# Kernel optimization log

Measured on AMD Instinct MI355X. Metric: run time of the kernel, lower is better.

Reference implementation:

```python
import jax, jax.numpy as jnp
import numpy as np

B, N, DIN, DOUT = 16, 256, 64, 64
TEMP = 2.0          # temperatures[0]
POOL_K = 0.5        # pool_ratios[0]
BN_EPS = 1e-5


def setup_inputs() -> dict:
    key = jax.random.key(0)
    ks = jax.random.split(key, 8)
    g = lambda i, shape: (jax.random.normal(ks[i], shape, jnp.float32) * 0.08)
    return {
        "x": jax.random.normal(ks[0], (B, N, DIN), jnp.float32),
        # GraphAttentionLayer params
        "W_att": g(1, (DIN, DOUT)), "b_att": jnp.zeros((DOUT,), jnp.float32),
        "att_w": g(2, (DOUT,)),                      # att_weight [DOUT,1] squeezed
        "W_pwa": g(3, (DIN, DOUT)), "b_pwa": jnp.zeros((DOUT,), jnp.float32),
        "W_pna": g(4, (DIN, DOUT)), "b_pna": jnp.zeros((DOUT,), jnp.float32),
        "bn_scale": jnp.ones((DOUT,), jnp.float32),
        "bn_bias": jnp.zeros((DOUT,), jnp.float32),
        # GraphPool params
        "pool_w": g(5, (DOUT,)), "pool_b": jnp.zeros((), jnp.float32),
    }


def reference(x, W_att, b_att, att_w, W_pwa, b_pwa, W_pna, b_pna,
              bn_scale, bn_bias, pool_w, pool_b):
    # --- GraphAttentionLayer (eval mode: dropout = identity) ---
    # pairwise node multiplication: [B, i, j, DIN]
    pm = x[:, :, None, :] * x[:, None, :, :]
    att = jnp.tanh(jnp.einsum('bijd,de->bije', pm, W_att) + b_att)   # [B,N,N,DOUT]
    logits = jnp.einsum('bije,e->bij', att, att_w) / TEMP            # [B,N,N]
    # torch softmax over dim=-2 of [B,i,j,1] == axis j (the aggregated axis)
    A = jax.nn.softmax(logits, axis=2)                               # [B,N,N]
    agg = jnp.einsum('bij,bjd->bid', A, x)                           # [B,N,DIN]
    h = (agg @ W_pwa + b_pwa) + (x @ W_pna + b_pna)                  # [B,N,DOUT]
    # BatchNorm1d eval with running_mean=0, running_var=1
    h = h * (bn_scale / jnp.sqrt(1.0 + BN_EPS)) + bn_bias
    h = jax.nn.selu(h)
    # --- GraphPool (eval mode: dropout = identity) ---
    scores = jax.nn.sigmoid(h @ pool_w + pool_b)                     # [B,N]
    k = max(int(N * POOL_K), 1)
    _, idx = jax.lax.top_k(scores, k)                                # [B,k]
    hw = h * scores[:, :, None]
    out = jnp.take_along_axis(hw, idx[:, :, None], axis=1)           # [B,k,DOUT]
    return out
```

## Files before the change

### kernel.cpp

```cpp
#include <hip/hip_runtime.h>
#include <hip/hip_bf16.h>
#include <math.h>

#define BB 16
#define NN 256
#define DD 64
#define KTOP 128

typedef short s16x8 __attribute__((ext_vector_type(8)));
typedef float f32x4 __attribute__((ext_vector_type(4)));

typedef union { s16x8 v; unsigned u[4]; } frag_u;
typedef union { __hip_bfloat162 b2; unsigned u; } cvu;

__device__ __forceinline__ float asf(unsigned u){ union{unsigned u;float f;}c; c.u=u; return c.f; }

__device__ __forceinline__ void split2(float v0, float v1, unsigned& hu, unsigned& lu) {
    cvu c; c.b2 = __float22bfloat162_rn(make_float2(v0, v1));
    unsigned h = c.u;
    float l0 = v0 - asf(h << 16);
    float l1 = v1 - asf(h & 0xffff0000u);
    c.b2 = __float22bfloat162_rn(make_float2(l0, l1));
    hu = h; lu = c.u;
}

__global__ __launch_bounds__(512, 6) void k_logits(
    const float* __restrict__ x, const float* __restrict__ W_att,
    const float* __restrict__ b_att, const float* __restrict__ att_w,
    float* __restrict__ U)
{
    const int ig = blockIdx.x;
    const int b  = blockIdx.y;
    const int tid = threadIdx.x;
    const int w = tid >> 6, lane = tid & 63;
    const int quad = lane >> 4, c16 = lane & 15;
    const int ibase = ig * 4;
    const int G = ig >> 3;
    const bool active = w < (8 - G);
    const int jb = (G + w) * 32;

    __shared__ s16x8 sB[2][2][4][2][64];
    __shared__ float sXi[4 * 64];
    __shared__ float sL[4][256];
    __shared__ float sBatt[64];
    __shared__ float sAww[64];

    if (tid < 256) sXi[tid] = x[(b * NN + ibase + (tid >> 6)) * DD + (tid & 63)];
    if (tid < 64) sBatt[tid] = b_att[tid];
    else if (tid < 128) sAww[tid - 64] = att_w[tid - 64];

    const float L2E2 = 2.8853900817779268f;

    float halfS;
    {
        float sa = 0.0f;
        #pragma unroll
        for (int mt = 0; mt < 4; ++mt) {
            float4 a4 = ((const float4*)att_w)[mt * 4 + quad];
            sa += (a4.x + a4.y) + (a4.z + a4.w);
        }
        sa += __shfl_xor(sa, 16);
        sa += __shfl_xor(sa, 32);
        halfS = 0.5f * sa;
    }

    const int bks = w >> 2, bmt = w & 3;

    frag_u Xh[2][2], Xl[2][2];
    if (active) {
        #pragma unroll
        for (int jt = 0; jt < 2; ++jt) {
            #pragma unroll
            for (int ks = 0; ks < 2; ++ks) {
                const float* xr = &x[(b * NN + jb + jt * 16 + c16) * DD + ks * 32 + quad * 8];
                float4 a0 = *(const float4*)xr;
                float4 a1 = *(const float4*)(xr + 4);
                split2(a0.x, a0.y, Xh[jt][ks].u[0], Xl[jt][ks].u[0]);
                split2(a0.z, a0.w, Xh[jt][ks].u[1], Xl[jt][ks].u[1]);
                split2(a1.x, a1.y, Xh[jt][ks].u[2], Xl[jt][ks].u[2]);
                split2(a1.z, a1.w, Xh[jt][ks].u[3], Xl[jt][ks].u[3]);
            }
        }
    }
    __syncthreads();

    {
        const float* xr = &sXi[0 * 64 + bks * 32 + quad * 8];
        float4 c0 = *(const float4*)xr;
        float4 c1 = *(const float4*)(xr + 4);
        float xiv[8] = {c0.x,c0.y,c0.z,c0.w,c1.x,c1.y,c1.z,c1.w};
        const float* wp = &W_att[(bks * 32 + quad * 8) * 64 + bmt * 16 + c16];
        frag_u bh, bl;
        split2(wp[0] * xiv[0], wp[64] * xiv[1], bh.u[0], bl.u[0]);
        split2(wp[128] * xiv[2], wp[192] * xiv[3], bh.u[1], bl.u[1]);
        split2(wp[256] * xiv[4], wp[320] * xiv[5], bh.u[2], bl.u[2]);
        split2(wp[384] * xiv[6], wp[448] * xiv[7], bh.u[3], bl.u[3]);
        sB[0][bks][bmt][0][lane] = bh.v;
        sB[0][bks][bmt][1][lane] = bl.v;
    }

    #pragma unroll
    for (int ii = 0; ii < 4; ++ii) {
        __syncthreads();

        if (ii < 3) {
            const float* xr = &sXi[(ii + 1) * 64 + bks * 32 + quad * 8];
            float4 c0 = *(const float4*)xr;
            float4 c1 = *(const float4*)(xr + 4);
            float xiv[8] = {c0.x,c0.y,c0.z,c0.w,c1.x,c1.y,c1.z,c1.w};
            const float* wp = &W_att[(bks * 32 + quad * 8) * 64 + bmt * 16 + c16];
            frag_u bh, bl;
            split2(wp[0] * xiv[0], wp[64] * xiv[1], bh.u[0], bl.u[0]);
            split2(wp[128] * xiv[2], wp[192] * xiv[3], bh.u[1], bl.u[1]);
            split2(wp[256] * xiv[4], wp[320] * xiv[5], bh.u[2], bl.u[2]);
            split2(wp[384] * xiv[6], wp[448] * xiv[7], bh.u[3], bl.u[3]);
            sB[(ii + 1) & 1][bks][bmt][0][lane] = bh.v;
            sB[(ii + 1) & 1][bks][bmt][1][lane] = bl.v;
        }

        if (active) {
            const int cur = ii & 1;
            float s0 = 0.0f, s1 = 0.0f;
            #pragma unroll
            for (int eth = 0; eth < 2; ++eth) {
                f32x4 acc[2][2];
                #pragma unroll
                for (int e2 = 0; e2 < 2; ++e2) {
                    f32x4 bi = *(const f32x4*)&sBatt[(eth * 2 + e2) * 16 + quad * 4];
                    acc[e2][0] = bi;
                    acc[e2][1] = bi;
                }
                #pragma unroll
                for (int ks = 0; ks < 2; ++ks) {
                    #pragma unroll
                    for (int e2 = 0; e2 < 2; ++e2) {
                        const int mt = eth * 2 + e2;
                        s16x8 ah = sB[cur][ks][mt][0][lane];
                        s16x8 al = sB[cur][ks][mt][1][lane];
                        #pragma unroll
                        for (int jt = 0; jt < 2; ++jt) {
                            acc[e2][jt] = __builtin_amdgcn_mfma_f32_16x16x32_bf16(ah, Xh[jt][ks].v, acc[e2][jt], 0, 0, 0);
                            acc[e2][jt] = __builtin_amdgcn_mfma_f32_16x16x32_bf16(al, Xh[jt][ks].v, acc[e2][jt], 0, 0, 0);
                            acc[e2][jt] = __builtin_amdgcn_mfma_f32_16x16x32_bf16(ah, Xl[jt][ks].v, acc[e2][jt], 0, 0, 0);
                        }
                    }
                }
                #pragma unroll
                for (int e2 = 0; e2 < 2; ++e2) {
                    const int mt = eth * 2 + e2;
                    f32x4 awwv = *(const f32x4*)&sAww[mt * 16 + quad * 4];
                    #pragma unroll
                    for (int r = 0; r < 4; ++r) {
                        {
                            float m = __builtin_amdgcn_exp2f(acc[e2][0][r] * L2E2);
                            s0 = fmaf(awwv[r], __builtin_amdgcn_rcpf(m + 1.0f), s0);
                        }
                        {
                            float m = __builtin_amdgcn_exp2f(acc[e2][1][r] * L2E2);
                            s1 = fmaf(awwv[r], __builtin_amdgcn_rcpf(m + 1.0f), s1);
                        }
                    }
                }
            }
            s0 += __shfl_xor(s0, 16);
            s0 += __shfl_xor(s0, 32);
            s1 += __shfl_xor(s1, 16);
            s1 += __shfl_xor(s1, 32);
            if (quad == 0) {
                sL[ii][jb + c16]      = halfS - s0;
                sL[ii][jb + 16 + c16] = halfS - s1;
            }
        }
    }
    __syncthreads();

    #pragma unroll
    for (int c = 0; c < 4; ++c) {
        float* Ur = &U[(b * NN + ibase + c) * NN];
        for (int j = ibase + tid; j < NN; j += 512) Ur[j] = sL[c][j];
    }
    {
        const int cnt = (NN - (ibase + 4)) * 4;
        for (int m = tid; m < cnt; m += 512) {
            int rr = ibase + 4 + (m >> 2);
            U[(b * NN + rr) * NN + ibase + (m & 3)] = sL[m & 3][rr];
        }
    }
}

__global__ __launch_bounds__(256) void k_soft(
    const float* __restrict__ x, const float* __restrict__ U,
    const float* __restrict__ Wpwa, const float* __restrict__ bpwa,
    const float* __restrict__ Wpna, const float* __restrict__ bpna,
    const float* __restrict__ bnsc, const float* __restrict__ bnbi,
    const float* __restrict__ poolw, const float* __restrict__ poolb,
    float* __restrict__ hbuf, float* __restrict__ scores)
{
    const int rg = blockIdx.x;
    const int b  = blockIdx.y;
    const int w = threadIdx.x >> 6, lane = threadIdx.x & 63;
    const int r = rg * 4 + w;

    __shared__ float sA[4][256];
    __shared__ float sAgg[4][64];
    __shared__ float sXi[4][64];

    const float* row = &U[(b * NN + r) * NN];
    float lg0 = row[lane], lg1 = row[lane + 64], lg2 = row[lane + 128], lg3 = row[lane + 192];
    float m = fmaxf(fmaxf(lg0, lg1), fmaxf(lg2, lg3));
    #pragma unroll
    for (int off = 32; off; off >>= 1) m = fmaxf(m, __shfl_xor(m, off));
    float e0 = __expf(lg0 - m), e1 = __expf(lg1 - m), e2 = __expf(lg2 - m), e3 = __expf(lg3 - m);
    float ssum = e0 + e1 + e2 + e3;
    #pragma unroll
    for (int off = 32; off; off >>= 1) ssum += __shfl_xor(ssum, off);
    float inv = 1.0f / ssum;
    sA[w][lane] = e0 * inv; sA[w][lane + 64] = e1 * inv;
    sA[w][lane + 128] = e2 * inv; sA[w][lane + 192] = e3 * inv;
    sXi[w][lane] = x[(b * NN + r) * DD + lane];
    __asm__ volatile("s_waitcnt lgkmcnt(0)" ::: "memory");

    float ag0 = 0.f, ag1 = 0.f, ag2 = 0.f, ag3 = 0.f;
    const float4* A4 = (const float4*)&sA[w][0];
    const float* xb = &x[(b * NN) * DD];
    #pragma unroll 8
    for (int jq = 0; jq < 64; ++jq) {
        float4 a = A4[jq];
        int j = jq * 4;
        ag0 = fmaf(a.x, xb[(j + 0) * DD + lane], ag0);
        ag1 = fmaf(a.y, xb[(j + 1) * DD + lane], ag1);
        ag2 = fmaf(a.z, xb[(j + 2) * DD + lane], ag2);
        ag3 = fmaf(a.w, xb[(j + 3) * DD + lane], ag3);
    }
    sAgg[w][lane] = (ag0 + ag1) + (ag2 + ag3);
    __asm__ volatile("s_waitcnt lgkmcnt(0)" ::: "memory");

    double hacc = (double)bpwa[lane] + (double)bpna[lane];
    #pragma unroll 4
    for (int d = 0; d < 64; ++d) {
        hacc += (double)sAgg[w][d] * (double)Wpwa[d * DD + lane]
              + (double)sXi[w][d]  * (double)Wpna[d * DD + lane];
    }
    const double bnmul = 0.99999500003749968750e0;
    double hb = hacc * ((double)bnsc[lane] * bnmul) + (double)bnbi[lane];
    float hf = (float)hb;
    const float LAM = 1.0507009873554805f, ALP = 1.6732632423543772f;
    float hs = hf > 0.0f ? LAM * hf : LAM * ALP * (__expf(hf) - 1.0f);
    hbuf[(b * NN + r) * DD + lane] = hs;

    double z = (double)hs * (double)poolw[lane];
    #pragma unroll
    for (int off = 32; off; off >>= 1) z += __shfl_xor(z, off);
    if (lane == 0) {
        double zz = z + (double)poolb[0];
        scores[b * NN + r] = (float)(1.0 / (1.0 + exp(-zz)));
    }
}

__global__ __launch_bounds__(256) void k_topk(
    const float* __restrict__ scores, const float* __restrict__ hbuf,
    float* __restrict__ out)
{
    const int c = blockIdx.x;
    const int b = blockIdx.y;
    const int t = threadIdx.x;
    __shared__ float ss[256];
    __shared__ int   perm[16];
    ss[t] = scores[b * NN + t];
    __syncthreads();
    const float my = ss[t];
    int rank = 0;
    #pragma unroll 8
    for (int j = 0; j < 256; ++j) {
        float v = ss[j];
        rank += (v > my) || (v == my && j < t);
    }
    if ((rank >> 4) == c) perm[rank & 15] = t;
    __syncthreads();
    #pragma unroll
    for (int m = t; m < 16 * DD; m += 256) {
        int r = m >> 6, e = m & 63;
        int i = perm[r];
        out[(b * KTOP + c * 16 + r) * DD + e] = hbuf[(b * NN + i) * DD + e] * ss[i];
    }
}

extern "C" void kernel_launch(void* const* d_in, const int* in_sizes, int n_in,
                              void* d_out, int out_size, void* d_ws, size_t ws_size,
                              hipStream_t stream) {
    const float* x        = (const float*)d_in[0];
    const float* W_att    = (const float*)d_in[1];
    const float* b_att    = (const float*)d_in[2];
    const float* att_w    = (const float*)d_in[3];
    const float* W_pwa    = (const float*)d_in[4];
    const float* b_pwa    = (const float*)d_in[5];
    const float* W_pna    = (const float*)d_in[6];
    const float* b_pna    = (const float*)d_in[7];
    const float* bn_scale = (const float*)d_in[8];
    const float* bn_bias  = (const float*)d_in[9];
    const float* pool_w   = (const float*)d_in[10];
    const float* pool_b   = (const float*)d_in[11];

    float* U       = (float*)d_ws;
    float* hbuf    = U + BB * NN * NN;
    float* scoresW = hbuf + BB * NN * DD;
    float* out     = (float*)d_out;

    k_logits<<<dim3(64, BB), 512, 0, stream>>>(x, W_att, b_att, att_w, U);
    k_soft<<<dim3(64, BB), 256, 0, stream>>>(x, U, W_pwa, b_pwa, W_pna, b_pna,
                                             bn_scale, bn_bias, pool_w, pool_b,
                                             hbuf, scoresW);
    k_topk<<<dim3(8, BB), 256, 0, stream>>>(scoresW, hbuf, out);
}
```

Before: 148.6 us.

## Drop strided symmetric-fill writes in logits kernel; read transposed entries in softmax

k_logits stops writing the mirrored lower-triangle entries of the symmetric logits matrix, which it used to scatter with strided 4-float stores. k_soft now handles 8 rows per 512-thread block and stages the needed columns of earlier rows (an 8-wide float4 slice per prior row) in shared memory. It uses those values in place of the unwritten lower-triangle entries. The double-precision projection loop is also split into four independent accumulators to shorten the dependency chain, which changes the summation order slightly.

```diff
diff --git a/kernel.cpp b/kernel.cpp
--- a/kernel.cpp
+++ b/kernel.cpp
@@ -179,16 +179,9 @@
         float* Ur = &U[(b * NN + ibase + c) * NN];
         for (int j = ibase + tid; j < NN; j += 512) Ur[j] = sL[c][j];
     }
-    {
-        const int cnt = (NN - (ibase + 4)) * 4;
-        for (int m = tid; m < cnt; m += 512) {
-            int rr = ibase + 4 + (m >> 2);
-            U[(b * NN + rr) * NN + ibase + (m & 3)] = sL[m & 3][rr];
-        }
-    }
-}
-
-__global__ __launch_bounds__(256) void k_soft(
+}
+
+__global__ __launch_bounds__(512) void k_soft(
     const float* __restrict__ x, const float* __restrict__ U,
     const float* __restrict__ Wpwa, const float* __restrict__ bpwa,
     const float* __restrict__ Wpna, const float* __restrict__ bpna,
@@ -196,28 +189,48 @@
     const float* __restrict__ poolw, const float* __restrict__ poolb,
     float* __restrict__ hbuf, float* __restrict__ scores)
 {
-    const int rg = blockIdx.x;
-    const int b  = blockIdx.y;
-    const int w = threadIdx.x >> 6, lane = threadIdx.x & 63;
-    const int r = rg * 4 + w;
-
-    __shared__ float sA[4][256];
-    __shared__ float sAgg[4][64];
-    __shared__ float sXi[4][64];
+    const int rg8 = blockIdx.x;
+    const int b   = blockIdx.y;
+    const int tid = threadIdx.x;
+    const int w = tid >> 6, lane = tid & 63;
+    const int rbase8 = rg8 * 8;
+    const int r = rbase8 + w;
+    const int rbase4 = r & ~3;
+
+    __shared__ float sLow[256][9];
+    __shared__ float sA[8][256];
+    __shared__ float sAgg[8][64];
+    __shared__ float sXi[8][64];
+
+    if (tid < rbase8 + 4) {
+        const float* uj = &U[(b * NN + tid) * NN + rbase8];
+        float4 u0 = *(const float4*)uj;
+        float4 u1 = *(const float4*)(uj + 4);
+        sLow[tid][0] = u0.x; sLow[tid][1] = u0.y; sLow[tid][2] = u0.z; sLow[tid][3] = u0.w;
+        sLow[tid][4] = u1.x; sLow[tid][5] = u1.y; sLow[tid][6] = u1.z; sLow[tid][7] = u1.w;
+    }
+    sXi[tid >> 6][tid & 63] = x[(b * NN + rbase8 + (tid >> 6)) * DD + (tid & 63)];
+    __syncthreads();
 
     const float* row = &U[(b * NN + r) * NN];
-    float lg0 = row[lane], lg1 = row[lane + 64], lg2 = row[lane + 128], lg3 = row[lane + 192];
-    float m = fmaxf(fmaxf(lg0, lg1), fmaxf(lg2, lg3));
+    float lg[4];
+    #pragma unroll
+    for (int k = 0; k < 4; ++k) {
+        int jj = lane + 64 * k;
+        float gv = row[jj];
+        float lv = sLow[jj][w];
+        lg[k] = (jj >= rbase4) ? gv : lv;
+    }
+    float m = fmaxf(fmaxf(lg[0], lg[1]), fmaxf(lg[2], lg[3]));
     #pragma unroll
     for (int off = 32; off; off >>= 1) m = fmaxf(m, __shfl_xor(m, off));
-    float e0 = __expf(lg0 - m), e1 = __expf(lg1 - m), e2 = __expf(lg2 - m), e3 = __expf(lg3 - m);
-    float ssum = e0 + e1 + e2 + e3;
+    float e0 = __expf(lg[0] - m), e1 = __expf(lg[1] - m), e2 = __expf(lg[2] - m), e3 = __expf(lg[3] - m);
+    float ssum = (e0 + e1) + (e2 + e3);
     #pragma unroll
     for (int off = 32; off; off >>= 1) ssum += __shfl_xor(ssum, off);
     float inv = 1.0f / ssum;
     sA[w][lane] = e0 * inv; sA[w][lane + 64] = e1 * inv;
     sA[w][lane + 128] = e2 * inv; sA[w][lane + 192] = e3 * inv;
-    sXi[w][lane] = x[(b * NN + r) * DD + lane];
     __asm__ volatile("s_waitcnt lgkmcnt(0)" ::: "memory");
 
     float ag0 = 0.f, ag1 = 0.f, ag2 = 0.f, ag3 = 0.f;
@@ -235,12 +248,19 @@
     sAgg[w][lane] = (ag0 + ag1) + (ag2 + ag3);
     __asm__ volatile("s_waitcnt lgkmcnt(0)" ::: "memory");
 
-    double hacc = (double)bpwa[lane] + (double)bpna[lane];
+    double h0 = 0.0, h1 = 0.0, h2 = 0.0, h3 = 0.0;
     #pragma unroll 4
-    for (int d = 0; d < 64; ++d) {
-        hacc += (double)sAgg[w][d] * (double)Wpwa[d * DD + lane]
-              + (double)sXi[w][d]  * (double)Wpna[d * DD + lane];
-    }
+    for (int d = 0; d < 64; d += 4) {
+        h0 += (double)sAgg[w][d + 0] * (double)Wpwa[(d + 0) * DD + lane]
+            + (double)sXi[w][d + 0]  * (double)Wpna[(d + 0) * DD + lane];
+        h1 += (double)sAgg[w][d + 1] * (double)Wpwa[(d + 1) * DD + lane]
+            + (double)sXi[w][d + 1]  * (double)Wpna[(d + 1) * DD + lane];
+        h2 += (double)sAgg[w][d + 2] * (double)Wpwa[(d + 2) * DD + lane]
+            + (double)sXi[w][d + 2]  * (double)Wpna[(d + 2) * DD + lane];
+        h3 += (double)sAgg[w][d + 3] * (double)Wpwa[(d + 3) * DD + lane]
+            + (double)sXi[w][d + 3]  * (double)Wpna[(d + 3) * DD + lane];
+    }
+    double hacc = ((double)bpwa[lane] + (double)bpna[lane]) + ((h0 + h1) + (h2 + h3));
     const double bnmul = 0.99999500003749968750e0;
     double hb = hacc * ((double)bnsc[lane] * bnmul) + (double)bnbi[lane];
     float hf = (float)hb;
@@ -307,7 +327,7 @@
     float* out     = (float*)d_out;
 
     k_logits<<<dim3(64, BB), 512, 0, stream>>>(x, W_att, b_att, att_w, U);
-    k_soft<<<dim3(64, BB), 256, 0, stream>>>(x, U, W_pwa, b_pwa, W_pna, b_pna,
+    k_soft<<<dim3(32, BB), 512, 0, stream>>>(x, U, W_pwa, b_pwa, W_pna, b_pna,
                                              bn_scale, bn_bias, pool_w, pool_b,
                                              hbuf, scoresW);
     k_topk<<<dim3(8, BB), 256, 0, stream>>>(scoresW, hbuf, out);
```

Result: slower. 153.0 us (+2.9%).
